# Optimization experiments

Measured on AMD Instinct MI355X. Metric: run time of the kernel, lower is better.

Reference implementation:

```python
import jax, jax.numpy as jnp
import numpy as np

GRID_SIZE = 16
SPLINE_ORDER = 4
GRID_LO, GRID_HI = -1.0, 1.0
NUM_GRID = 2 * SPLINE_ORDER + GRID_SIZE + 1  # 25 knots
NUM_COEFFS = GRID_SIZE + SPLINE_ORDER        # 20 basis functions
B, IN_F, OUT_F = 2048, 512, 512


def _make_grid():
    h = (GRID_HI - GRID_LO) / GRID_SIZE
    t1 = -SPLINE_ORDER * h + GRID_LO
    t2 = (GRID_SIZE + SPLINE_ORDER + 1) * h + GRID_LO
    return jnp.linspace(t1, t2, NUM_GRID)


def _bspline_basis(x, grid):
    # x: [..., in]; returns [..., in, NUM_COEFFS] via De Boor recursion
    xe = x[..., None]
    bases = ((xe >= grid[:-1]) & (xe < grid[1:])).astype(x.dtype)
    for k in range(1, SPLINE_ORDER + 1):
        left = (xe - grid[:-k - 1]) / (grid[k:-1] - grid[:-k - 1]) * bases[..., :-1]
        right = (grid[k + 1:] - xe) / (grid[k + 1:] - grid[1:-k]) * bases[..., 1:]
        bases = left + right
    return bases


def setup_inputs() -> dict:
    key = jax.random.key(0)
    ks = jax.random.split(key, 5)
    fan = np.sqrt(1.0 / IN_F)
    return {
        "x": jax.random.normal(ks[0], (B, IN_F), jnp.float32),
        "prelu_weight": jax.random.normal(ks[1], (OUT_F, IN_F), jnp.float32) * 0.25,
        "base_weight": jax.random.uniform(ks[2], (OUT_F, IN_F), jnp.float32, -fan, fan),
        "spline_weight": jax.random.uniform(ks[3], (OUT_F, IN_F), jnp.float32, -fan, fan),
        "spline_coeffs": jax.random.normal(ks[4], (OUT_F, IN_F, NUM_COEFFS), jnp.float32) * 0.1,
    }


def reference(x, prelu_weight, base_weight, spline_weight, spline_coeffs):
    grid = _make_grid()
    xc = jnp.clip(x, GRID_LO, GRID_HI)
    pos = jax.nn.relu(xc)
    neg = xc - pos
    # base path: sum_j base_w[i,j]*(prelu_w[i,j]*neg[b,j] + pos[b,j])
    # fused: never materialize the [out, B, in] prelu output
    base = neg @ (base_weight * prelu_weight).T + pos @ base_weight.T  # [B, out]
    basis = _bspline_basis(xc, grid)  # [B, in, K]
    # spline path: fold spline_weight into coeffs, single contraction over (j,k)
    eff_coeffs = spline_weight[:, :, None] * spline_coeffs  # [out, in, K]
    spline = jnp.einsum('bjk,ijk->bi', basis, eff_coeffs)   # [B, out]
    return base + spline
```

## Files before the change

kernel.cpp:

```cpp
#include <hip/hip_runtime.h>


typedef _Float16 half_t;
typedef __attribute__((ext_vector_type(8))) _Float16 half8;
typedef __attribute__((ext_vector_type(4))) float floatx4;

#define B_DIM   2048
#define J_DIM   512
#define O_DIM   512
#define SLOTS   22
#define K_TOT   (J_DIM * SLOTS)
#define MTILE   128
#define NTILE   128
#define BK      32
#define KSPLIT  8
#define KS_LEN  (K_TOT / KSPLIT)
#define KCH     (KS_LEN / BK)

__device__ __forceinline__ void bspline5(float xc, int& k0, float Nv[5]) {
    const float invS = 7.68f;
    float u = (xc + 1.5f) * invS;
    int m = (int)u;
    m = min(max(m, 3), 19);
    k0 = m - 4;
    Nv[0] = 1.f; Nv[1] = 0.f; Nv[2] = 0.f; Nv[3] = 0.f; Nv[4] = 0.f;
#pragma unroll
    for (int d = 1; d <= 4; ++d) {
        float nw[5];
        float inv_d = 1.0f / (float)d;
#pragma unroll
        for (int r = 0; r < 5; ++r) {
            if (r > d) { nw[r] = 0.f; continue; }
            float kk = (float)(m - d + r);
            float acc = 0.f;
            if (r >= 1) acc += (u - kk) * Nv[r - 1];
            if (r < d)  acc += (kk + (float)(d + 1) - u) * Nv[r];
            nw[r] = acc * inv_d;
        }
#pragma unroll
        for (int r = 0; r < 5; ++r) Nv[r] = nw[r];
    }
}

__global__ __launch_bounds__(256) void prep_A(const float* __restrict__ x,
                                              half_t* __restrict__ A) {
    __shared__ half_t rec[J_DIM * SLOTS];
    int b = blockIdx.x;
    int t = threadIdx.x;
#pragma unroll
    for (int jj = 0; jj < 2; ++jj) {
        int j = t + jj * 256;
        float xv = x[(size_t)b * J_DIM + j];
        float xc = fminf(fmaxf(xv, -1.f), 1.f);
        float pos = fmaxf(xc, 0.f);
        float neg = xc - pos;
        int k0; float Nv[5];
        bspline5(xc, k0, Nv);
        half_t* r = rec + j * SLOTS;
#pragma unroll
        for (int k = 0; k < 20; ++k) r[k] = (half_t)0.f;
#pragma unroll
        for (int rr = 0; rr < 5; ++rr) {
            int k = k0 + rr;
            if (k >= 0) r[k] = (half_t)Nv[rr];
        }
        r[20] = (half_t)neg;
        r[21] = (half_t)pos;
    }
    __syncthreads();
    const uint4* src = (const uint4*)rec;
    uint4* dst = (uint4*)(A + (size_t)b * K_TOT);
    for (int i = t; i < (J_DIM * SLOTS * 2) / 16; i += 256) dst[i] = src[i];
}

__global__ __launch_bounds__(256) void prep_C(const float* __restrict__ pw,
                                              const float* __restrict__ bw,
                                              const float* __restrict__ sw,
                                              const float* __restrict__ sc,
                                              half_t* __restrict__ Ct) {
    __shared__ half_t rec[J_DIM * SLOTS];
    int i = blockIdx.x;
    int t = threadIdx.x;
#pragma unroll
    for (int jj = 0; jj < 2; ++jj) {
        int j = t + jj * 256;
        size_t ij = (size_t)i * J_DIM + j;
        float s = sw[ij], b = bw[ij], p = pw[ij];
        const float* scp = sc + ij * 20;
        half_t* r = rec + j * SLOTS;
#pragma unroll
        for (int k = 0; k < 20; ++k) r[k] = (half_t)(s * scp[k]);
        r[20] = (half_t)(b * p);
        r[21] = (half_t)b;
    }
    __syncthreads();
    const uint4* src = (const uint4*)rec;
    uint4* dst = (uint4*)(Ct + (size_t)i * K_TOT);
    for (int idx = t; idx < (J_DIM * SLOTS * 2) / 16; idx += 256) dst[idx] = src[idx];
}

__global__ __launch_bounds__(256) void gemm_f16(const half_t* __restrict__ A,
                                                const half_t* __restrict__ Bt,
                                                float* __restrict__ out) {
    __shared__ half_t As[MTILE * BK];
    __shared__ half_t Bs[NTILE * BK];

    int m0 = blockIdx.x * MTILE;
    int n0 = blockIdx.y * NTILE;
    int ks = blockIdx.z * KS_LEN;

    int t = threadIdx.x;
    int w = t >> 6;
    int l = t & 63;
    int wm = w >> 1, wn = w & 1;

    floatx4 acc[4][4] = {};

    int lrow = l >> 2;
    int lkof = (l & 3) * 8;

    const half_t* gA = A + (size_t)m0 * K_TOT + ks;
    const half_t* gB = Bt + (size_t)n0 * K_TOT + ks;

    int q = l >> 4;
    int fr = l & 15;

    for (int c = 0; c < KCH; ++c) {
        int kb = c * BK;
#pragma unroll
        for (int n = 0; n < 2; ++n) {
            int r = (w * 2 + n) * 16 + lrow;
            __builtin_amdgcn_global_load_lds(
                (const __attribute__((address_space(1))) unsigned int*)
                    (gA + (size_t)r * K_TOT + kb + lkof),
                (__attribute__((address_space(3))) unsigned int*)
                    (As + (w * 2 + n) * 512),
                16, 0, 0);
            __builtin_amdgcn_global_load_lds(
                (const __attribute__((address_space(1))) unsigned int*)
                    (gB + (size_t)r * K_TOT + kb + lkof),
                (__attribute__((address_space(3))) unsigned int*)
                    (Bs + (w * 2 + n) * 512),
                16, 0, 0);
        }
        __syncthreads();

        half8 af[4], bf[4];
#pragma unroll
        for (int mt = 0; mt < 4; ++mt)
            af[mt] = *(const half8*)(As + (wm * 64 + mt * 16 + fr) * BK + q * 8);
#pragma unroll
        for (int nt = 0; nt < 4; ++nt)
            bf[nt] = *(const half8*)(Bs + (wn * 64 + nt * 16 + fr) * BK + q * 8);
#pragma unroll
        for (int mt = 0; mt < 4; ++mt)
#pragma unroll
            for (int nt = 0; nt < 4; ++nt)
                acc[mt][nt] = __builtin_amdgcn_mfma_f32_16x16x32_f16(
                    af[mt], bf[nt], acc[mt][nt], 0, 0, 0);
        __syncthreads();
    }

#pragma unroll
    for (int mt = 0; mt < 4; ++mt)
#pragma unroll
        for (int nt = 0; nt < 4; ++nt) {
            int rr = m0 + wm * 64 + mt * 16 + q * 4;
            int cc = n0 + wn * 64 + nt * 16 + fr;
#pragma unroll
            for (int r = 0; r < 4; ++r)
                atomicAdd(out + (size_t)(rr + r) * O_DIM + cc, acc[mt][nt][r]);
        }
}

__global__ __launch_bounds__(256) void kan_fallback(const float* __restrict__ x,
                                                    const float* __restrict__ pw,
                                                    const float* __restrict__ bw,
                                                    const float* __restrict__ sw,
                                                    const float* __restrict__ sc,
                                                    float* __restrict__ out) {
    __shared__ float s_neg[J_DIM], s_pos[J_DIM], s_bas[J_DIM][5];
    __shared__ int s_k0[J_DIM];
    int b = blockIdx.x;
    int t = threadIdx.x;
#pragma unroll
    for (int jj = 0; jj < 2; ++jj) {
        int j = t + jj * 256;
        float xv = x[(size_t)b * J_DIM + j];
        float xc = fminf(fmaxf(xv, -1.f), 1.f);
        float pos = fmaxf(xc, 0.f);
        s_pos[j] = pos;
        s_neg[j] = xc - pos;
        int k0; float Nv[5];
        bspline5(xc, k0, Nv);
        s_k0[j] = k0;
#pragma unroll
        for (int r = 0; r < 5; ++r) s_bas[j][r] = Nv[r];
    }
    __syncthreads();
    for (int i = t; i < O_DIM; i += 256) {
        float acc = 0.f;
        for (int j = 0; j < J_DIM; ++j) {
            size_t ij = (size_t)i * J_DIM + j;
            float bwv = bw[ij];
            acc += bwv * (pw[ij] * s_neg[j] + s_pos[j]);
            int k0 = s_k0[j];
            const float* cp = sc + ij * 20;
            float sp = 0.f;
#pragma unroll
            for (int r = 0; r < 5; ++r) {
                int k = k0 + r;
                if (k >= 0) sp += s_bas[j][r] * cp[k];
            }
            acc += sw[ij] * sp;
        }
        out[(size_t)b * O_DIM + i] = acc;
    }
}

extern "C" void kernel_launch(void* const* d_in, const int* in_sizes, int n_in,
                              void* d_out, int out_size, void* d_ws, size_t ws_size,
                              hipStream_t stream) {
    const float* x  = (const float*)d_in[0];
    const float* pw = (const float*)d_in[1];
    const float* bw = (const float*)d_in[2];
    const float* sw = (const float*)d_in[3];
    const float* sc = (const float*)d_in[4];
    float* out = (float*)d_out;

    const size_t ws_needed = (size_t)(B_DIM + O_DIM) * K_TOT * sizeof(half_t);
    if (ws_size < ws_needed) {
        kan_fallback<<<B_DIM, 256, 0, stream>>>(x, pw, bw, sw, sc, out);
        return;
    }

    half_t* A  = (half_t*)d_ws;
    half_t* Ct = A + (size_t)B_DIM * K_TOT;

    hipMemsetAsync(d_out, 0, (size_t)out_size * sizeof(float), stream);
    prep_A<<<B_DIM, 256, 0, stream>>>(x, A);
    prep_C<<<O_DIM, 256, 0, stream>>>(pw, bw, sw, sc, Ct);
    dim3 g(B_DIM / MTILE, O_DIM / NTILE, KSPLIT);
    gemm_f16<<<g, 256, 0, stream>>>(A, Ct, out);
}
```

Before: 151.2 us.

## Fuse memset and prep kernels, swizzle LDS, and raise GEMM split-K

Merges the output zeroing, prep_C and prep_A into a single launch with block-range dispatch, which removes two launches and the memset. The GEMM now applies an XOR swizzle to the LDS k-offset on both the global_load_lds write side and the fragment read side to cut bank conflicts. It also doubles the split-K factor to 16 and adds a min-blocks-per-CU launch bound to raise occupancy. In exchange, the larger split-K doubles the number of fp32 atomic adds to the output.

```diff
diff --git a/kernel.cpp b/kernel.cpp
--- a/kernel.cpp
+++ b/kernel.cpp
@@ -13,9 +13,10 @@
 #define MTILE   128
 #define NTILE   128
 #define BK      32
-#define KSPLIT  8
+#define KSPLIT  16
 #define KS_LEN  (K_TOT / KSPLIT)
 #define KCH     (KS_LEN / BK)
+#define ZERO_BLKS 64
 
 __device__ __forceinline__ void bspline5(float xc, int& k0, float Nv[5]) {
     const float invS = 7.68f;
@@ -42,11 +43,49 @@
     }
 }
 
-__global__ __launch_bounds__(256) void prep_A(const float* __restrict__ x,
-                                              half_t* __restrict__ A) {
+__global__ __launch_bounds__(256) void prep_all(const float* __restrict__ x,
+                                                const float* __restrict__ pw,
+                                                const float* __restrict__ bw,
+                                                const float* __restrict__ sw,
+                                                const float* __restrict__ sc,
+                                                half_t* __restrict__ A,
+                                                half_t* __restrict__ Ct,
+                                                float* __restrict__ out) {
     __shared__ half_t rec[J_DIM * SLOTS];
-    int b = blockIdx.x;
+    int bid = blockIdx.x;
     int t = threadIdx.x;
+
+    if (bid < ZERO_BLKS) {
+        float4* o = (float4*)out;
+        int base = bid * 4096;
+#pragma unroll
+        for (int i = 0; i < 16; ++i)
+            o[base + i * 256 + t] = make_float4(0.f, 0.f, 0.f, 0.f);
+        return;
+    }
+
+    if (bid < ZERO_BLKS + O_DIM) {
+        int i = bid - ZERO_BLKS;
+#pragma unroll
+        for (int jj = 0; jj < 2; ++jj) {
+            int j = t + jj * 256;
+            size_t ij = (size_t)i * J_DIM + j;
+            float s = sw[ij], b = bw[ij], p = pw[ij];
+            const float* scp = sc + ij * 20;
+            half_t* r = rec + j * SLOTS;
+#pragma unroll
+            for (int k = 0; k < 20; ++k) r[k] = (half_t)(s * scp[k]);
+            r[20] = (half_t)(b * p);
+            r[21] = (half_t)b;
+        }
+        __syncthreads();
+        const uint4* src = (const uint4*)rec;
+        uint4* dst = (uint4*)(Ct + (size_t)i * K_TOT);
+        for (int idx = t; idx < (J_DIM * SLOTS * 2) / 16; idx += 256) dst[idx] = src[idx];
+        return;
+    }
+
+    int b = bid - ZERO_BLKS - O_DIM;
 #pragma unroll
     for (int jj = 0; jj < 2; ++jj) {
         int j = t + jj * 256;
@@ -73,35 +112,9 @@
     for (int i = t; i < (J_DIM * SLOTS * 2) / 16; i += 256) dst[i] = src[i];
 }
 
-__global__ __launch_bounds__(256) void prep_C(const float* __restrict__ pw,
-                                              const float* __restrict__ bw,
-                                              const float* __restrict__ sw,
-                                              const float* __restrict__ sc,
-                                              half_t* __restrict__ Ct) {
-    __shared__ half_t rec[J_DIM * SLOTS];
-    int i = blockIdx.x;
-    int t = threadIdx.x;
-#pragma unroll
-    for (int jj = 0; jj < 2; ++jj) {
-        int j = t + jj * 256;
-        size_t ij = (size_t)i * J_DIM + j;
-        float s = sw[ij], b = bw[ij], p = pw[ij];
-        const float* scp = sc + ij * 20;
-        half_t* r = rec + j * SLOTS;
-#pragma unroll
-        for (int k = 0; k < 20; ++k) r[k] = (half_t)(s * scp[k]);
-        r[20] = (half_t)(b * p);
-        r[21] = (half_t)b;
-    }
-    __syncthreads();
-    const uint4* src = (const uint4*)rec;
-    uint4* dst = (uint4*)(Ct + (size_t)i * K_TOT);
-    for (int idx = t; idx < (J_DIM * SLOTS * 2) / 16; idx += 256) dst[idx] = src[idx];
-}
-
-__global__ __launch_bounds__(256) void gemm_f16(const half_t* __restrict__ A,
-                                                const half_t* __restrict__ Bt,
-                                                float* __restrict__ out) {
+__global__ __launch_bounds__(256, 4) void gemm_f16(const half_t* __restrict__ A,
+                                                   const half_t* __restrict__ Bt,
+                                                   float* __restrict__ out) {
     __shared__ half_t As[MTILE * BK];
     __shared__ half_t Bs[NTILE * BK];
 
@@ -117,13 +130,14 @@
     floatx4 acc[4][4] = {};
 
     int lrow = l >> 2;
-    int lkof = (l & 3) * 8;
+    int lkof = (((l & 3) ^ ((l >> 3) & 3)) * 8);
 
     const half_t* gA = A + (size_t)m0 * K_TOT + ks;
     const half_t* gB = Bt + (size_t)n0 * K_TOT + ks;
 
     int q = l >> 4;
     int fr = l & 15;
+    int qs = (q ^ ((fr >> 1) & 3)) * 8;
 
     for (int c = 0; c < KCH; ++c) {
         int kb = c * BK;
@@ -148,10 +162,10 @@
         half8 af[4], bf[4];
 #pragma unroll
         for (int mt = 0; mt < 4; ++mt)
-            af[mt] = *(const half8*)(As + (wm * 64 + mt * 16 + fr) * BK + q * 8);
+            af[mt] = *(const half8*)(As + (wm * 64 + mt * 16 + fr) * BK + qs);
 #pragma unroll
         for (int nt = 0; nt < 4; ++nt)
-            bf[nt] = *(const half8*)(Bs + (wn * 64 + nt * 16 + fr) * BK + q * 8);
+            bf[nt] = *(const half8*)(Bs + (wn * 64 + nt * 16 + fr) * BK + qs);
 #pragma unroll
         for (int mt = 0; mt < 4; ++mt)
 #pragma unroll
@@ -237,9 +251,7 @@
     half_t* A  = (half_t*)d_ws;
     half_t* Ct = A + (size_t)B_DIM * K_TOT;
 
-    hipMemsetAsync(d_out, 0, (size_t)out_size * sizeof(float), stream);
-    prep_A<<<B_DIM, 256, 0, stream>>>(x, A);
-    prep_C<<<O_DIM, 256, 0, stream>>>(pw, bw, sw, sc, Ct);
+    prep_all<<<ZERO_BLKS + O_DIM + B_DIM, 256, 0, stream>>>(x, pw, bw, sw, sc, A, Ct, out);
     dim3 g(B_DIM / MTILE, O_DIM / NTILE, KSPLIT);
     gemm_f16<<<g, 256, 0, stream>>>(A, Ct, out);
 }
```

After: 159.6 us. 5.6% more time.
